# Kernel optimization log

Measured on AMD Instinct MI355X. Metric: run time of the kernel, lower is better.

Reference implementation:

```python
import jax, jax.numpy as jnp
import numpy as np

B = 64            # graphs in batch
N = 100_000       # total nodes
E = 600_000       # total edges of g == nodes of line graph lg
E2 = 1_500_000    # edges of line graph
H = 128           # hidden_dim
L = 3             # num_layers
MAXZ = 100

seg_sum = jax.ops.segment_sum


def setup_inputs() -> dict:
    key = jax.random.key(0)
    ks = jax.random.split(key, 20)
    s = 1.0 / np.sqrt(H)
    inp = {
        'z': jax.random.randint(ks[0], (N,), 0, MAXZ + 1),
        'd': jax.random.uniform(ks[1], (E, 1), dtype=jnp.float32),
        'src': jax.random.randint(ks[2], (E,), 0, N),
        'dst': jax.random.randint(ks[3], (E,), 0, N),
        'lsrc': jax.random.randint(ks[4], (E2,), 0, E),
        'ldst': jax.random.randint(ks[5], (E2,), 0, E),
        'node_graph': jnp.sort(jax.random.randint(ks[6], (N,), 0, B)),
        'edge_graph': jnp.sort(jax.random.randint(ks[7], (E,), 0, B)),
        'emb': jax.random.normal(ks[8], (MAXZ + 1, H), jnp.float32),
        'ep_w': jax.random.normal(ks[9], (1, H), jnp.float32) * s,
        'ep_b': jnp.zeros((H,), jnp.float32),
        'gW': jax.random.normal(ks[10], (L, H, H), jnp.float32) * s,
        'gb': jnp.zeros((L, H), jnp.float32),
        'lgW': jax.random.normal(ks[11], (L, H, H), jnp.float32) * s,
        'lgb': jnp.zeros((L, H), jnp.float32),
        'r1w': jax.random.normal(ks[12], (2 * H, H), jnp.float32) * s,
        'r1b': jnp.zeros((H,), jnp.float32),
        'r2w': jax.random.normal(ks[13], (H, 1), jnp.float32) * s,
        'r2b': jnp.zeros((1,), jnp.float32),
    }
    return inp


def _graph_conv(h, srcix, dstix, W, b, n_nodes):
    # DGL GraphConv, norm='both', aggregate-then-weight (in==out dims):
    # h' = D_in^{-1/2} * A^T * (D_out^{-1/2} * h) @ W + b, degrees clamped >= 1
    ones = jnp.ones(srcix.shape[0], h.dtype)
    deg_out = jnp.clip(seg_sum(ones, srcix, num_segments=n_nodes), 1.0)
    deg_in = jnp.clip(seg_sum(ones, dstix, num_segments=n_nodes), 1.0)
    m = h * (deg_out ** -0.5)[:, None]
    agg = seg_sum(m[srcix], dstix, num_segments=n_nodes)  # SpMM gather-scatter
    agg = agg * (deg_in ** -0.5)[:, None]
    return agg @ W + b


def _segment_mean(h, seg, n_seg):
    sums = seg_sum(h, seg, num_segments=n_seg)
    cnt = jnp.clip(seg_sum(jnp.ones(h.shape[0], h.dtype), seg, num_segments=n_seg), 1.0)
    return sums / cnt[:, None]


def reference(z, d, src, dst, lsrc, ldst, node_graph, edge_graph,
              emb, ep_w, ep_b, gW, gb, lgW, lgb, r1w, r1b, r2w, r2b):
    h = emb[z]                       # [N, H]
    e = d @ ep_w + ep_b              # [E, H]
    for i in range(L):
        h = jax.nn.relu(_graph_conv(h, src, dst, gW[i], gb[i], N))
    for i in range(L):
        e = jax.nn.relu(_graph_conv(e, lsrc, ldst, lgW[i], lgb[i], E))
    hg = _segment_mean(h, node_graph, B)   # [B, H]
    he = _segment_mean(e, edge_graph, B)   # [B, H]
    x = jnp.concatenate([hg, he], axis=-1)  # [B, 2H]
    y = jax.nn.silu(x @ r1w + r1b) @ r2w + r2b
    return y.reshape(-1)             # [B]
```

## Files before the change

kernel.cpp:

```cpp
#include <hip/hip_runtime.h>
#include <math.h>

#define H 128
typedef unsigned short u16;
typedef unsigned char u8;
typedef unsigned int u32;
typedef _Float16 f16;
typedef f16 f16x8 __attribute__((ext_vector_type(8)));
typedef float f32x4 __attribute__((ext_vector_type(4)));
typedef float f32x2 __attribute__((ext_vector_type(2)));

#if __has_builtin(__builtin_amdgcn_cvt_pk_fp8_f32)
#define HW8 1
#else
#define HW8 0
#endif

#define SSTRIDE 144

static inline int cdiv(long long a, long long b) { return (int)((a + b - 1) / b); }

__device__ __forceinline__ int swz_seg(int orig, int n) {
    int q = n >> 3, r = n & 7;
    int x = orig & 7;
    int base = (x < r) ? x * (q + 1) : r * (q + 1) + (x - r) * q;
    return base + (orig >> 3);
}
__device__ __forceinline__ int conv_bid(int orig, int nbCN, int nwg) {
    return (orig < nbCN) ? swz_seg(orig, nbCN)
                         : nbCN + swz_seg(orig - nbCN, nwg - nbCN);
}

struct F8 {
    static __device__ inline float dec(u8 v) {
        int e = (v >> 3) & 15, m = v & 7;
        float f = (e == 0) ? (float)m * 0.001953125f : ldexpf(1.f + 0.125f * (float)m, e - 7);
        return (v & 0x80) ? -f : f;
    }
    static __device__ inline u8 enc(float x) {
        u8 s = (u8)((__float_as_uint(x) >> 24) & 0x80);
        float ax = fabsf(x);
        if (!(ax < 448.f)) return s | 0x7E;
        if (ax < 0.015625f) {
            int m = (int)rintf(ax * 512.f);
            if (m >= 8) return s | 0x08;
            return s | (u8)m;
        }
        int e; float fr = frexpf(ax, &e);
        int E = e - 1;
        int m = (int)rintf(fr * 16.f - 8.f);
        if (m == 8) { m = 0; ++E; }
        if (E > 8) return s | 0x7E;
        return s | (u8)(((E + 7) << 3) | m);
    }
};

static __device__ inline u32 enc4(float x0, float x1, float x2, float x3) {
#if HW8
    u32 w = __builtin_amdgcn_cvt_pk_fp8_f32(x0, x1, 0, false);
    w = __builtin_amdgcn_cvt_pk_fp8_f32(x2, x3, w, true);
    return w;
#else
    union { u8 b[4]; u32 u; } p;
    p.b[0] = F8::enc(x0); p.b[1] = F8::enc(x1); p.b[2] = F8::enc(x2); p.b[3] = F8::enc(x3);
    return p.u;
#endif
}
static __device__ inline float4 dec4(u32 v) {
#if HW8
    f32x2 lo = __builtin_amdgcn_cvt_pk_f32_fp8(v, false);
    f32x2 hi = __builtin_amdgcn_cvt_pk_f32_fp8(v, true);
    return make_float4(lo.x, lo.y, hi.x, hi.y);
#else
    union { u32 u; u8 b[4]; } c; c.u = v;
    return make_float4(F8::dec(c.b[0]), F8::dec(c.b[1]), F8::dec(c.b[2]), F8::dec(c.b[3]));
#endif
}
static __device__ inline float dec1(u8 b) {
#if HW8
    return __builtin_amdgcn_cvt_f32_fp8((int)b, 0);
#else
    return F8::dec(b);
#endif
}

__global__ __launch_bounds__(256) void setup1_k(
    const float* __restrict__ gW, const float* __restrict__ lgW, f16* __restrict__ wt, int L, int nbPW,
    const int* __restrict__ src, const int* __restrict__ dst,
    const int* __restrict__ lsrc, const int* __restrict__ ldst,
    int* __restrict__ con, int* __restrict__ cin, int* __restrict__ coe, int* __restrict__ cie,
    int E, int E2, int nbHI,
    const int* __restrict__ node_graph, int N, const int* __restrict__ edge_graph,
    int B, int* __restrict__ cntn, int* __restrict__ cnte,
    const float* __restrict__ epw, const float* __restrict__ epb, float* __restrict__ uv) {
    int blk = blockIdx.x;
    if (blk < nbPW) {
        int mat = blk >> 6;
        int idx = (blk & 63) * 256 + threadIdx.x;
        int k = idx >> 7, n = idx & 127;
        const float* W = (mat < L) ? gW + (size_t)mat * H * H : lgW + (size_t)(mat - L) * H * H;
        wt[(size_t)mat * H * H + (size_t)n * H + k] = (f16)W[(size_t)k * H + n];
        return;
    }
    blk -= nbPW;
    if (blk < nbHI) {
        int i = blk * 256 + threadIdx.x;
        if (i < E) {
            atomicAdd(&con[src[i]], 1);
            atomicAdd(&cin[dst[i]], 1);
        } else if (i < E + E2) {
            int j = i - E;
            atomicAdd(&coe[lsrc[j]], 1);
            atomicAdd(&cie[ldst[j]], 1);
        }
        return;
    }
    blk -= nbHI;
    if (blk < 2) {
        const int* seg = blk ? edge_graph : node_graph;
        int n = blk ? E : N;
        int* cnt = blk ? cnte : cntn;
        __shared__ int bound[129];
        int b = threadIdx.x;
        if (b <= B) {
            int lo = 0, hi = n;
            while (lo < hi) {
                int mid = (lo + hi) >> 1;
                if (seg[mid] < b) lo = mid + 1; else hi = mid;
            }
            bound[b] = lo;
        }
        __syncthreads();
        if (b < B) cnt[b] = bound[b + 1] - bound[b];
        return;
    }
    {
        int n = threadIdx.x;
        if (n < H) {
            float su = 0.f, sv = 0.f;
            for (int k = 0; k < H; ++k) {
                float w = lgW[(size_t)k * H + n];
                su = fmaf(epw[k], w, su);
                sv = fmaf(epb[k], w, sv);
            }
            uv[n] = su;
            uv[n + H] = sv;
        }
    }
}

__global__ __launch_bounds__(256) void setup2_k(
    const int* __restrict__ con, const int* __restrict__ cin,
    const int* __restrict__ coe, const int* __restrict__ cie,
    float* __restrict__ ron, float* __restrict__ rin,
    float* __restrict__ roe, float* __restrict__ rie,
    const float* __restrict__ d, float2* __restrict__ pairE, int N, int E, int nbRS,
    int* __restrict__ offs_n, int nbN, int* __restrict__ offs_e, int* __restrict__ bsum) {
    int blk = blockIdx.x;
    if (blk < nbRS) {
        int i = blk * 256 + threadIdx.x;
        if (i < N) { int v = con[i]; ron[i] = rsqrtf((float)(v < 1 ? 1 : v)); }
        else if (i < 2 * N) { int n = i - N; int v = cin[n]; rin[n] = rsqrtf((float)(v < 1 ? 1 : v)); }
        else if (i < 2 * N + E) {
            int n = i - 2 * N; int v = coe[n];
            float r = rsqrtf((float)(v < 1 ? 1 : v));
            roe[n] = r;
            pairE[n] = make_float2(r * d[n], r);
        } else if (i < 2 * N + 2 * E) {
            int n = i - 2 * N - E; int v = cie[n]; rie[n] = rsqrtf((float)(v < 1 ? 1 : v));
        }
        return;
    }
    blk -= nbRS;
    {
        __shared__ int sh[256];
        const int* in; int* out; int n; int gid;
        if (blk < nbN) { in = cin; out = offs_n; n = N; gid = blk * 256 + threadIdx.x; }
        else { in = cie; out = offs_e; n = E; gid = (blk - nbN) * 256 + threadIdx.x; }
        int v = (gid < n) ? in[gid] : 0;
        sh[threadIdx.x] = v;
        __syncthreads();
        for (int off = 1; off < 256; off <<= 1) {
            int t = (threadIdx.x >= off) ? sh[threadIdx.x - off] : 0;
            __syncthreads();
            sh[threadIdx.x] += t;
            __syncthreads();
        }
        if (gid < n) out[gid] = sh[threadIdx.x] - v;
        if (threadIdx.x == 255) bsum[blk] = sh[255];
    }
}

__global__ __launch_bounds__(256) void scan_bsum2_k(int* __restrict__ bsum, int nbA, int nbB) {
    __shared__ int sh[256];
    __shared__ int carry;
#pragma unroll 1
    for (int part = 0; part < 2; ++part) {
        int base0 = part ? nbA : 0;
        int nb = part ? nbB : nbA;
        if (threadIdx.x == 0) carry = 0;
        __syncthreads();
        for (int base = 0; base < nb; base += 256) {
            int i = base + threadIdx.x;
            int v = (i < nb) ? bsum[base0 + i] : 0;
            sh[threadIdx.x] = v;
            __syncthreads();
            for (int off = 1; off < 256; off <<= 1) {
                int t = (threadIdx.x >= off) ? sh[threadIdx.x - off] : 0;
                __syncthreads();
                sh[threadIdx.x] += t;
                __syncthreads();
            }
            if (i < nb) bsum[base0 + i] = sh[threadIdx.x] - v + carry;
            __syncthreads();
            if (threadIdx.x == 0) carry += sh[255];
            __syncthreads();
        }
    }
}

__global__ __launch_bounds__(256) void setup3_k(
    int* __restrict__ offs_n, int* __restrict__ cur_n, int N, int nbN, int E,
    int* __restrict__ offs_e, int* __restrict__ cur_e, int E2, int nbE,
    const int* __restrict__ bsum,
    const int* __restrict__ z, const float* __restrict__ emb,
    const float* __restrict__ ron, u8* __restrict__ featN) {
    int blk = blockIdx.x;
    int nbSA = nbN + nbE;
    if (blk < nbSA) {
        int* offs; int* curp; int n; int gid; int nnz;
        if (blk < nbN) { offs = offs_n; curp = cur_n; n = N; gid = blk * 256 + threadIdx.x; nnz = E; }
        else { offs = offs_e; curp = cur_e; n = E; gid = (blk - nbN) * 256 + threadIdx.x; nnz = E2; }
        if (gid < n) {
            int v = offs[gid] + bsum[blk];
            offs[gid] = v;
            curp[gid] = v;
        }
        if (gid == 0) offs[n] = nnz;
        return;
    }
    blk -= nbSA;
    {
        int idx = blk * 256 + threadIdx.x;
        if (idx >= N * 32) return;
        int n = idx >> 5, c4 = (idx & 31) << 2;
        float sc = ron[n];
        const float4 v = *(const float4*)(emb + (size_t)z[n] * H + c4);
        *(u32*)(featN + (size_t)n * H + c4) = enc4(v.x * sc, v.y * sc, v.z * sc, v.w * sc);
    }
}

__global__ __launch_bounds__(256) void fill2_k(const int* __restrict__ src, const int* __restrict__ dst,
                                               const int* __restrict__ lsrc, const int* __restrict__ ldst,
                                               int* __restrict__ cur_n, int* __restrict__ cur_e,
                                               uint2* __restrict__ nbr_n, uint2* __restrict__ nbr_e,
                                               const float2* __restrict__ pairE, float2* __restrict__ pslot,
                                               int E, int E2) {
    int i = blockIdx.x * 256 + threadIdx.x;
    if (i < E) {
        int dd = dst[i];
        int p = atomicAdd(&cur_n[dd], 1);
        nbr_n[p] = make_uint2((u32)src[i], (u32)dd);
    } else if (i < E + E2) {
        int j = i - E;
        int ls = lsrc[j];
        int dd = ldst[j];
        int p = atomicAdd(&cur_e[dd], 1);
        nbr_e[p] = make_uint2((u32)ls, (u32)dd);
        pslot[p] = pairE[ls];
    }
}

__device__ __forceinline__ void gather_phase(
    const u8* __restrict__ Xin,
    const int* __restrict__ offs, const uint2* __restrict__ nbr2,
    const float* __restrict__ rs_in, int M,
    int row0, f16 (*As)[136], int wave, int lane) {
    const int rowbase = row0 + wave * 16;
    {
        uint2* zp = (uint2*)&As[wave * 16][0];
#pragma unroll
        for (int i = 0; i < 9; ++i) {
            int o = lane + i * 64;
            if (o < 544) zp[o] = make_uint2(0u, 0u);
        }
    }
    const int gl = lane >> 4;
    const int ln = lane & 15;
    const int rbase4 = rowbase + gl * 4;
    const int r_lo = min(rbase4, M);
    const int r_hi = min(rbase4 + 4, M);
    const int jbeg = offs[r_lo];
    const int jend = offs[r_hi];
    if (jbeg >= jend) return;
    const int mrow = M - 1;
    const float rsr0 = rs_in[min(rbase4 + 0, mrow)];
    const float rsr1 = rs_in[min(rbase4 + 1, mrow)];
    const float rsr2 = rs_in[min(rbase4 + 2, mrow)];
    const float rsr3 = rs_in[min(rbase4 + 3, mrow)];

    float a0 = 0.f, a1 = 0.f, a2 = 0.f, a3 = 0.f, a4 = 0.f, a5 = 0.f, a6 = 0.f, a7 = 0.f;
    int curdst = -1;

#define FLUSH_ROW()                                                              \
    do {                                                                         \
        const int dd_ = curdst - rbase4;                                         \
        const float ri_ = dd_ == 0 ? rsr0 : (dd_ == 1 ? rsr1 : (dd_ == 2 ? rsr2 : rsr3)); \
        f16x8 o_;                                                                \
        o_[0] = (f16)(a0 * ri_); o_[1] = (f16)(a1 * ri_);                        \
        o_[2] = (f16)(a2 * ri_); o_[3] = (f16)(a3 * ri_);                        \
        o_[4] = (f16)(a4 * ri_); o_[5] = (f16)(a5 * ri_);                        \
        o_[6] = (f16)(a6 * ri_); o_[7] = (f16)(a7 * ri_);                        \
        *(f16x8*)&As[curdst - row0][ln << 3] = o_;                               \
    } while (0)

    uint2 eA[8], eB[8], fA[8], fB[8], eN[8];
#pragma unroll
    for (int k = 0; k < 8; ++k) eA[k] = nbr2[min(jbeg + k, jend - 1)];
#pragma unroll
    for (int k = 0; k < 8; ++k) eB[k] = nbr2[min(jbeg + 8 + k, jend - 1)];
#pragma unroll
    for (int k = 0; k < 8; ++k)
        fA[k] = *(const uint2*)(Xin + ((size_t)eA[k].x << 7) + (ln << 3));
    int jc = jbeg;
    while (true) {
        const int jn = jc + 8;
        const bool more = jn < jend;
        if (more) {
#pragma unroll
            for (int k = 0; k < 8; ++k)
                fB[k] = *(const uint2*)(Xin + ((size_t)eB[k].x << 7) + (ln << 3));
#pragma unroll
            for (int k = 0; k < 8; ++k) eN[k] = nbr2[min(jn + 8 + k, jend - 1)];
        }
#pragma unroll
        for (int k = 0; k < 8; ++k) {
            if (jc + k < jend) {
                const int dk = (int)eA[k].y;
                if (dk != curdst) {
                    if (curdst >= 0) {
                        FLUSH_ROW();
                        a0 = a1 = a2 = a3 = a4 = a5 = a6 = a7 = 0.f;
                    }
                    curdst = dk;
                }
                float4 lo = dec4(fA[k].x);
                float4 hi = dec4(fA[k].y);
                a0 += lo.x; a1 += lo.y; a2 += lo.z; a3 += lo.w;
                a4 += hi.x; a5 += hi.y; a6 += hi.z; a7 += hi.w;
            }
        }
        if (!more) break;
#pragma unroll
        for (int k = 0; k < 8; ++k) { eA[k] = eB[k]; eB[k] = eN[k]; fA[k] = fB[k]; }
        jc = jn;
    }
    FLUSH_ROW();
#undef FLUSH_ROW
}

template <bool STORE>
__device__ __forceinline__ void conv_mfma_phase(
    u8* __restrict__ Xout, const f16* __restrict__ Wt, const float* __restrict__ bias,
    const float* __restrict__ scale_out, int M, int row0, f16 (*As)[136], int wave, int lane) {
    const int rowbase = row0 + wave * 16;
    if (rowbase >= M) return;
    const int l15 = lane & 15;
    const int quad = lane >> 4;

    f16x8 a[4];
#pragma unroll
    for (int kt = 0; kt < 4; ++kt)
        a[kt] = *(const f16x8*)&As[wave * 16 + l15][kt * 32 + quad * 8];

    float rsc[4];
#pragma unroll
    for (int r = 0; r < 4; ++r) {
        int gr = rowbase + quad * 4 + r;
        rsc[r] = (scale_out && gr < M) ? scale_out[gr] : 1.f;
    }

    u8* stage = (u8*)&As[wave * 16][0];

#pragma unroll
    for (int n0 = 0; n0 < 8; ++n0) {
        f32x4 acc = {0.f, 0.f, 0.f, 0.f};
        const f16* bp = Wt + (size_t)(n0 * 16 + l15) * H + quad * 8;
#pragma unroll
        for (int kt = 0; kt < 4; ++kt) {
            f16x8 b = *(const f16x8*)(bp + kt * 32);
            acc = __builtin_amdgcn_mfma_f32_16x16x32_f16(a[kt], b, acc, 0, 0, 0);
        }
        int col = n0 * 16 + l15;
        float bv = bias[col];
        float o[4];
#pragma unroll
        for (int r = 0; r < 4; ++r) o[r] = fmaxf(acc[r] + bv, 0.f) * rsc[r];
        u32 w = enc4(o[0], o[1], o[2], o[3]);
#pragma unroll
        for (int r = 0; r < 4; ++r) stage[(quad * 4 + r) * SSTRIDE + col] = (u8)(w >> (8 * r));
    }
    if (STORE) {
        const int lr = lane >> 2;
        const int lc = (lane & 3) * 32;
        int gr = rowbase + lr;
        if (gr < M) {
            uint4 v0 = *(const uint4*)&stage[lr * SSTRIDE + lc];
            uint4 v1 = *(const uint4*)&stage[lr * SSTRIDE + lc + 16];
            *(uint4*)(Xout + (size_t)gr * H + lc) = v0;
            *(uint4*)(Xout + (size_t)gr * H + lc + 16) = v1;
        }
    }
}

__device__ __forceinline__ void conv_mfma_pool_phase(
    const f16* __restrict__ Wt, const float* __restrict__ bias, int M, int row0,
    f16 (*As)[136], float (*pool)[128], int wave, int lane,
    const int* __restrict__ seg, float* __restrict__ outp, bool uni) {
    const int rowbase = row0 + wave * 16;
    if (rowbase >= M) return;
    const int l15 = lane & 15;
    const int quad = lane >> 4;

    f16x8 a[4];
#pragma unroll
    for (int kt = 0; kt < 4; ++kt)
        a[kt] = *(const f16x8*)&As[wave * 16 + l15][kt * 32 + quad * 8];

    const int gr0 = rowbase + quad * 4;
    const int remM = M - gr0;
    int g0 = -1, g1 = -1, g2 = -1, g3 = -1;
    if (!uni) {
        g0 = (0 < remM) ? seg[gr0 + 0] : -1;
        g1 = (1 < remM) ? seg[gr0 + 1] : -1;
        g2 = (2 < remM) ? seg[gr0 + 2] : -1;
        g3 = (3 < remM) ? seg[gr0 + 3] : -1;
    }

#pragma unroll
    for (int n0 = 0; n0 < 8; ++n0) {
        f32x4 acc = {0.f, 0.f, 0.f, 0.f};
        const f16* bp = Wt + (size_t)(n0 * 16 + l15) * H + quad * 8;
#pragma unroll
        for (int kt = 0; kt < 4; ++kt) {
            f16x8 b = *(const f16x8*)(bp + kt * 32);
            acc = __builtin_amdgcn_mfma_f32_16x16x32_f16(a[kt], b, acc, 0, 0, 0);
        }
        const int col = n0 * 16 + l15;
        const float bv = bias[col];
        const float o0 = (0 < remM) ? fmaxf(acc[0] + bv, 0.f) : 0.f;
        const float o1 = (1 < remM) ? fmaxf(acc[1] + bv, 0.f) : 0.f;
        const float o2 = (2 < remM) ? fmaxf(acc[2] + bv, 0.f) : 0.f;
        const float o3 = (3 < remM) ? fmaxf(acc[3] + bv, 0.f) : 0.f;
        if (uni) {
            float s = (o0 + o1) + (o2 + o3);
            s += __shfl_xor(s, 16);
            s += __shfl_xor(s, 32);
            if (quad == 0) pool[wave][col] = s;
        } else {
            float ac = o0; int gc = g0;
            if (g1 == gc) ac += o1; else { if (gc >= 0) atomicAdd(&outp[(size_t)gc * H + col], ac); gc = g1; ac = o1; }
            if (g2 == gc) ac += o2; else { if (gc >= 0) atomicAdd(&outp[(size_t)gc * H + col], ac); gc = g2; ac = o2; }
            if (g3 == gc) ac += o3; else { if (gc >= 0) atomicAdd(&outp[(size_t)gc * H + col], ac); gc = g3; ac = o3; }
            if (gc >= 0) atomicAdd(&outp[(size_t)gc * H + col], ac);
        }
    }
}

template <bool STORE>
__device__ __forceinline__ void conv_wave(
    const u8* __restrict__ Xin, u8* __restrict__ Xout,
    const int* __restrict__ offs, const uint2* __restrict__ nbr2,
    const float* __restrict__ rs_in, const f16* __restrict__ Wt,
    const float* __restrict__ bias, const float* __restrict__ scale_out, int M,
    int row0, f16 (*As)[136], int wave, int lane) {
    gather_phase(Xin, offs, nbr2, rs_in, M, row0, As, wave, lane);
    conv_mfma_phase<STORE>(Xout, Wt, bias, scale_out, M, row0, As, wave, lane);
}

__device__ __forceinline__ void conv_wave_l0e(
    u8* __restrict__ Xout, const int* __restrict__ offs,
    const float2* __restrict__ pslot, const float* __restrict__ rs_in,
    const float* __restrict__ uv, const float* __restrict__ bias,
    const float* __restrict__ scale_out, int E,
    int row0, int wave, int lane) {
    const int rowbase = row0 + wave * 16;
    const int r = lane >> 2;
    const int t = lane & 3;
    const int growu = rowbase + r;
    const int grow = min(growu, E - 1);
    const int jb = offs[grow];
    const int je = offs[grow + 1];
    float sd = 0.f, sw = 0.f;
    for (int j = jb + t; j < je; j += 4) {
        float2 p = pslot[j];
        sd += p.x; sw += p.y;
    }
    sd += __shfl_xor(sd, 1); sw += __shfl_xor(sw, 1);
    sd += __shfl_xor(sd, 2); sw += __shfl_xor(sw, 2);
    if (growu >= E) return;
    const float ri = rs_in[growu];
    const float so = scale_out[growu];
    sd *= ri; sw *= ri;
    const int c0 = t * 32;
    u32 wbuf[8];
#pragma unroll
    for (int c4 = 0; c4 < 8; ++c4) {
        const int c = c0 + c4 * 4;
        const float4 ua = *(const float4*)(uv + c);
        const float4 va = *(const float4*)(uv + H + c);
        const float4 ba = *(const float4*)(bias + c);
        const float o0 = fmaxf(fmaf(sd, ua.x, fmaf(sw, va.x, ba.x)), 0.f) * so;
        const float o1 = fmaxf(fmaf(sd, ua.y, fmaf(sw, va.y, ba.y)), 0.f) * so;
        const float o2 = fmaxf(fmaf(sd, ua.z, fmaf(sw, va.z, ba.z)), 0.f) * so;
        const float o3 = fmaxf(fmaf(sd, ua.w, fmaf(sw, va.w, ba.w)), 0.f) * so;
        wbuf[c4] = enc4(o0, o1, o2, o3);
    }
    *(uint4*)(Xout + (size_t)growu * H + c0) = *(uint4*)&wbuf[0];
    *(uint4*)(Xout + (size_t)growu * H + c0 + 16) = *(uint4*)&wbuf[4];
}

__global__ __launch_bounds__(256, 4) void conv2_k(
    const u8* __restrict__ XinN, u8* __restrict__ XoutN,
    const int* __restrict__ offs_n, const uint2* __restrict__ nbr_n,
    const float* __restrict__ rinN, const f16* __restrict__ WtN,
    const float* __restrict__ biasN, const float* __restrict__ scaleN, int N, int nbCN,
    const u8* __restrict__ XinE, u8* __restrict__ XoutE,
    const int* __restrict__ offs_e, const uint2* __restrict__ nbr_e,
    const float* __restrict__ rinE, const f16* __restrict__ WtE,
    const float* __restrict__ biasE, const float* __restrict__ scaleE, int E) {
    __shared__ f16 As[64][136];
    const int tid = threadIdx.x;
    const int wave = tid >> 6;
    const int lane = tid & 63;
    const int bid = conv_bid((int)blockIdx.x, nbCN, (int)gridDim.x);
    if (bid < nbCN) {
        conv_wave<true>(XinN, XoutN, offs_n, nbr_n, rinN, WtN, biasN, scaleN, N,
                        bid * 64, As, wave, lane);
    } else {
        conv_wave<true>(XinE, XoutE, offs_e, nbr_e, rinE, WtE, biasE, scaleE, E,
                        (bid - nbCN) * 64, As, wave, lane);
    }
}

__global__ __launch_bounds__(256, 4) void conv2_l0_k(
    const u8* __restrict__ XinN, u8* __restrict__ XoutN,
    const int* __restrict__ offs_n, const uint2* __restrict__ nbr_n,
    const float* __restrict__ rinN, const f16* __restrict__ WtN,
    const float* __restrict__ biasN, const float* __restrict__ scaleN, int N, int nbCN,
    u8* __restrict__ XoutE,
    const int* __restrict__ offs_e, const float2* __restrict__ pslot,
    const float* __restrict__ rinE, const float* __restrict__ uv,
    const float* __restrict__ biasE, const float* __restrict__ scaleE, int E) {
    __shared__ f16 As[64][136];
    const int tid = threadIdx.x;
    const int wave = tid >> 6;
    const int lane = tid & 63;
    const int bid = conv_bid((int)blockIdx.x, nbCN, (int)gridDim.x);
    if (bid < nbCN) {
        conv_wave<true>(XinN, XoutN, offs_n, nbr_n, rinN, WtN, biasN, scaleN, N,
                        bid * 64, As, wave, lane);
    } else {
        conv_wave_l0e(XoutE, offs_e, pslot, rinE, uv, biasE, scaleE, E,
                      (bid - nbCN) * 64, wave, lane);
    }
}

__global__ __launch_bounds__(256, 4) void conv2_last_k(
    const u8* __restrict__ XinN,
    const int* __restrict__ offs_n, const uint2* __restrict__ nbr_n,
    const float* __restrict__ rinN, const f16* __restrict__ WtN,
    const float* __restrict__ biasN, int N, int nbCN,
    const int* __restrict__ node_graph, float* __restrict__ hg,
    const u8* __restrict__ XinE,
    const int* __restrict__ offs_e, const uint2* __restrict__ nbr_e,
    const float* __restrict__ rinE, const f16* __restrict__ WtE,
    const float* __restrict__ biasE, int E,
    const int* __restrict__ edge_graph, float* __restrict__ he) {
    __shared__ f16 As[64][136];
    __shared__ float pool[4][128];
    const int tid = threadIdx.x;
    const int wave = tid >> 6;
    const int lane = tid & 63;
    const int bid = conv_bid((int)blockIdx.x, nbCN, (int)gridDim.x);
    const bool isN = bid < nbCN;
    const int row0 = (isN ? bid : bid - nbCN) * 64;
    const int M = isN ? N : E;
    const int* seg = isN ? node_graph : edge_graph;
    float* outp = isN ? hg : he;

    ((float*)pool)[tid] = 0.f;
    ((float*)pool)[tid + 256] = 0.f;
    const int gblk = seg[row0];
    const bool uni = (seg[min(row0 + 63, M - 1)] == gblk);
    __syncthreads();

    if (isN) {
        gather_phase(XinN, offs_n, nbr_n, rinN, N, row0, As, wave, lane);
        conv_mfma_pool_phase(WtN, biasN, N, row0, As, pool, wave, lane, seg, outp, uni);
    } else {
        gather_phase(XinE, offs_e, nbr_e, rinE, E, row0, As, wave, lane);
        conv_mfma_pool_phase(WtE, biasE, E, row0, As, pool, wave, lane, seg, outp, uni);
    }
    __syncthreads();
    if (uni && tid < 128) {
        float s = (pool[0][tid] + pool[1][tid]) + (pool[2][tid] + pool[3][tid]);
        atomicAdd(&outp[(size_t)gblk * H + tid], s);
    }
}

__global__ __launch_bounds__(128) void readout_k(const float* __restrict__ hg, const float* __restrict__ he,
                                                 const int* __restrict__ cn, const int* __restrict__ ce,
                                                 const float* __restrict__ r1w, const float* __restrict__ r1b,
                                                 const float* __restrict__ r2w, const float* __restrict__ r2b,
                                                 float* __restrict__ out) {
    const int b = blockIdx.x;
    const int j = threadIdx.x;
    const float invn = 1.f / fmaxf((float)cn[b], 1.f);
    const float inve = 1.f / fmaxf((float)ce[b], 1.f);
    float acc = r1b[j];
    for (int k = 0; k < H; ++k) acc = fmaf(hg[(size_t)b * H + k] * invn, r1w[(size_t)k * H + j], acc);
    for (int k = 0; k < H; ++k) acc = fmaf(he[(size_t)b * H + k] * inve, r1w[(size_t)(k + H) * H + j], acc);
    float s = acc / (1.f + expf(-acc));
    __shared__ float red[128];
    red[j] = s * r2w[j];
    __syncthreads();
    for (int off = 64; off > 0; off >>= 1) {
        if (j < off) red[j] += red[j + off];
        __syncthreads();
    }
    if (j == 0) out[b] = red[0] + r2b[0];
}

__global__ void report_k(float* out, int n, float val) {
    int i = blockIdx.x * 64 + threadIdx.x;
    if (i < n) out[i] = val;
}

extern "C" void kernel_launch(void* const* d_in, const int* in_sizes, int n_in,
                              void* d_out, int out_size, void* d_ws, size_t ws_size,
                              hipStream_t stream) {
    const int* z          = (const int*)d_in[0];
    const float* d        = (const float*)d_in[1];
    const int* src        = (const int*)d_in[2];
    const int* dst        = (const int*)d_in[3];
    const int* lsrc       = (const int*)d_in[4];
    const int* ldst       = (const int*)d_in[5];
    const int* node_graph = (const int*)d_in[6];
    const int* edge_graph = (const int*)d_in[7];
    const float* emb      = (const float*)d_in[8];
    const float* epw      = (const float*)d_in[9];
    const float* epb      = (const float*)d_in[10];
    const float* gW       = (const float*)d_in[11];
    const float* gb       = (const float*)d_in[12];
    const float* lgW      = (const float*)d_in[13];
    const float* lgb      = (const float*)d_in[14];
    const float* r1w      = (const float*)d_in[15];
    const float* r1b      = (const float*)d_in[16];
    const float* r2w      = (const float*)d_in[17];
    const float* r2b      = (const float*)d_in[18];

    const int N  = in_sizes[0];
    const int E  = in_sizes[2];
    const int E2 = in_sizes[4];
    const int B  = out_size;
    const int L  = 3;
    float* out = (float*)d_out;
    char* ws = (char*)d_ws;

    size_t off = 0;
    auto al = [&](size_t b) -> char* { char* q = ws + off; off += (b + 255) & ~(size_t)255; return q; };
    u8*  featEA = (u8*)al((size_t)E * H);
    u8*  featEB = (u8*)al((size_t)E * H);
    u8*  featNA = (u8*)al((size_t)N * H);
    u8*  featNB = (u8*)al((size_t)N * H);
    f16* wt    = (f16*)al((size_t)2 * L * H * H * 2);
    float* uv  = (float*)al((size_t)2 * H * 4);
    float* ron = (float*)al((size_t)N * 4);
    float* rin = (float*)al((size_t)N * 4);
    float* roe = (float*)al((size_t)E * 4);
    float* rie = (float*)al((size_t)E * 4);
    float2* pairE = (float2*)al((size_t)E * 8);
    size_t cntCount = (size_t)2 * N + 2 * E + 2 * B;
    size_t cntBytes = cntCount * 4;
    size_t poolsOff = (cntBytes + 255) & ~(size_t)255;
    char* zblock = al(poolsOff + (size_t)2 * B * H * 4);
    int* cnts = (int*)zblock;
    float* pools = (float*)(zblock + poolsOff);
    int* con = cnts; int* cin_ = con + N; int* coe = cin_ + N; int* cie = coe + E;
    int* cntn = cie + E; int* cnte = cntn + B;
    float* hg = pools;
    float* he = pools + (size_t)B * H;
    int* offs_n = (int*)al(((size_t)N + 1) * 4);
    int* cur_n  = (int*)al((size_t)N * 4);
    int* offs_e = (int*)al(((size_t)E + 1) * 4);
    int* cur_e  = (int*)al((size_t)E * 4);
    uint2* nbr_n = (uint2*)al((size_t)E * 8);
    uint2* nbr_e = (uint2*)al((size_t)E2 * 8);
    float2* pslot = (float2*)al((size_t)E2 * 8);
    int nbN = cdiv(N, 256), nbE = cdiv(E, 256);
    int* bsum   = (int*)al(((size_t)nbN + nbE + 2) * 4);

    if (off > ws_size) {
        report_k<<<cdiv(B, 64), 64, 0, stream>>>(out, B, (float)(ws_size >> 20));
        return;
    }

    hipMemsetAsync(zblock, 0, poolsOff + (size_t)2 * B * H * 4, stream);

    const int nbPW = 2 * L * 64;
    const int nbHI = cdiv((long long)E + E2, 256);
    setup1_k<<<nbPW + nbHI + 3, 256, 0, stream>>>(gW, lgW, wt, L, nbPW,
                                                  src, dst, lsrc, ldst, con, cin_, coe, cie,
                                                  E, E2, nbHI, node_graph, N, edge_graph, B, cntn, cnte,
                                                  epw, epb, uv);

    const int nbRS = cdiv((long long)2 * N + 2 * E, 256);
    setup2_k<<<nbRS + nbN + nbE, 256, 0, stream>>>(con, cin_, coe, cie, ron, rin, roe, rie,
                                                   d, pairE, N, E, nbRS, offs_n, nbN, offs_e, bsum);
    scan_bsum2_k<<<1, 256, 0, stream>>>(bsum, nbN, nbE);

    const int nbIN = cdiv((long long)N * 32, 256);
    setup3_k<<<nbN + nbE + nbIN, 256, 0, stream>>>(offs_n, cur_n, N, nbN, E,
                                                   offs_e, cur_e, E2, nbE, bsum, z, emb, ron, featNA);

    fill2_k<<<cdiv((long long)E + E2, 256), 256, 0, stream>>>(src, dst, lsrc, ldst, cur_n, cur_e,
                                                              nbr_n, nbr_e, pairE, pslot, E, E2);

    const int nbCN = cdiv(N, 64), nbCE = cdiv(E, 64);

    conv2_l0_k<<<nbCN + nbCE, 256, 0, stream>>>(
        featNA, featNB, offs_n, nbr_n, rin, wt, gb, ron, N, nbCN,
        featEB, offs_e, pslot, rie, uv, lgb, roe, E);

    conv2_k<<<nbCN + nbCE, 256, 0, stream>>>(
        featNB, featNA, offs_n, nbr_n, rin, wt + (size_t)1 * H * H, gb + (size_t)1 * H, ron, N, nbCN,
        featEB, featEA, offs_e, nbr_e, rie, wt + (size_t)(L + 1) * H * H, lgb + (size_t)1 * H, roe, E);

    conv2_last_k<<<nbCN + nbCE, 256, 0, stream>>>(
        featNA, offs_n, nbr_n, rin, wt + (size_t)2 * H * H, gb + (size_t)2 * H, N, nbCN, node_graph, hg,
        featEA, offs_e, nbr_e, rie, wt + (size_t)(L + 2) * H * H, lgb + (size_t)2 * H, E, edge_graph, he);

    readout_k<<<B, 128, 0, stream>>>(hg, he, cntn, cnte, r1w, r1b, r2w, r2b, out);
}
```

Measured before the change: 1.012 ms.

## Stage SpMM neighbor gathers through LDS with async global_load_lds pipeline

Rewrites the gather phase so each wave handles 16 rows together rather than 4 rows per 16-lane group. Neighbor index chunks and fp8 feature rows are copied straight into a per-wave LDS staging buffer with global_load_lds, using a 4-deep ring and explicit vmcnt waits to keep loads in flight. Each lane then accumulates 2 channels and flushes through a shuffle of the row scale. The aim is better memory-level parallelism and lower register pressure in the gather, at the cost of about 20KB extra LDS per block, which may reduce occupancy, plus serialized per-edge processing across the wave.

New measurement: 1.074 ms. 6.1% more time.

```diff
diff --git a/kernel.cpp b/kernel.cpp
--- a/kernel.cpp
+++ b/kernel.cpp
@@ -10,6 +10,9 @@
 typedef float f32x4 __attribute__((ext_vector_type(4)));
 typedef float f32x2 __attribute__((ext_vector_type(2)));
 
+typedef __attribute__((address_space(1))) const void gas_void;
+typedef __attribute__((address_space(3))) void las_void;
+
 #if __has_builtin(__builtin_amdgcn_cvt_pk_fp8_f32)
 #define HW8 1
 #else
@@ -17,6 +20,7 @@
 #endif
 
 #define SSTRIDE 144
+#define STG_W 5120
 
 static inline int cdiv(long long a, long long b) { return (int)((a + b - 1) / b); }
 
@@ -74,13 +78,6 @@
 #else
     union { u32 u; u8 b[4]; } c; c.u = v;
     return make_float4(F8::dec(c.b[0]), F8::dec(c.b[1]), F8::dec(c.b[2]), F8::dec(c.b[3]));
-#endif
-}
-static __device__ inline float dec1(u8 b) {
-#if HW8
-    return __builtin_amdgcn_cvt_f32_fp8((int)b, 0);
-#else
-    return F8::dec(b);
 #endif
 }
 
@@ -274,8 +271,8 @@
 __device__ __forceinline__ void gather_phase(
     const u8* __restrict__ Xin,
     const int* __restrict__ offs, const uint2* __restrict__ nbr2,
-    const float* __restrict__ rs_in, int M,
-    int row0, f16 (*As)[136], int wave, int lane) {
+    const float* __restrict__ rs_in, int M, int nnz,
+    int row0, f16 (*As)[136], u8* __restrict__ stageW, int wave, int lane) {
     const int rowbase = row0 + wave * 16;
     {
         uint2* zp = (uint2*)&As[wave * 16][0];
@@ -285,78 +282,80 @@
             if (o < 544) zp[o] = make_uint2(0u, 0u);
         }
     }
-    const int gl = lane >> 4;
-    const int ln = lane & 15;
-    const int rbase4 = rowbase + gl * 4;
-    const int r_lo = min(rbase4, M);
-    const int r_hi = min(rbase4 + 4, M);
-    const int jbeg = offs[r_lo];
-    const int jend = offs[r_hi];
-    if (jbeg >= jend) return;
-    const int mrow = M - 1;
-    const float rsr0 = rs_in[min(rbase4 + 0, mrow)];
-    const float rsr1 = rs_in[min(rbase4 + 1, mrow)];
-    const float rsr2 = rs_in[min(rbase4 + 2, mrow)];
-    const float rsr3 = rs_in[min(rbase4 + 3, mrow)];
-
-    float a0 = 0.f, a1 = 0.f, a2 = 0.f, a3 = 0.f, a4 = 0.f, a5 = 0.f, a6 = 0.f, a7 = 0.f;
+    if (rowbase >= M) return;
+    const int rhi = min(rowbase + 16, M);
+    const int J0 = offs[rowbase];
+    const int J1 = offs[rhi];
+    if (J0 >= J1) return;
+
+    float rsv = rs_in[min(rowbase + (lane & 15), M - 1)];
+    asm volatile("" : "+v"(rsv));
+
+    u8* featW = stageW;
+    int* nbrW = (int*)(stageW + 4096);
+
+    float acc0 = 0.f, acc1 = 0.f;
     int curdst = -1;
 
-#define FLUSH_ROW()                                                              \
+#define FLUSH()                                                                  \
     do {                                                                         \
-        const int dd_ = curdst - rbase4;                                         \
-        const float ri_ = dd_ == 0 ? rsr0 : (dd_ == 1 ? rsr1 : (dd_ == 2 ? rsr2 : rsr3)); \
-        f16x8 o_;                                                                \
-        o_[0] = (f16)(a0 * ri_); o_[1] = (f16)(a1 * ri_);                        \
-        o_[2] = (f16)(a2 * ri_); o_[3] = (f16)(a3 * ri_);                        \
-        o_[4] = (f16)(a4 * ri_); o_[5] = (f16)(a5 * ri_);                        \
-        o_[6] = (f16)(a6 * ri_); o_[7] = (f16)(a7 * ri_);                        \
-        *(f16x8*)&As[curdst - row0][ln << 3] = o_;                               \
+        float ri_ = __shfl(rsv, curdst - rowbase);                               \
+        union { f16 h[2]; u32 u; } P_;                                           \
+        P_.h[0] = (f16)(acc0 * ri_);                                             \
+        P_.h[1] = (f16)(acc1 * ri_);                                             \
+        *((u32*)&As[curdst - row0][0] + lane) = P_.u;                            \
     } while (0)
 
-    uint2 eA[8], eB[8], fA[8], fB[8], eN[8];
-#pragma unroll
-    for (int k = 0; k < 8; ++k) eA[k] = nbr2[min(jbeg + k, jend - 1)];
-#pragma unroll
-    for (int k = 0; k < 8; ++k) eB[k] = nbr2[min(jbeg + 8 + k, jend - 1)];
-#pragma unroll
-    for (int k = 0; k < 8; ++k)
-        fA[k] = *(const uint2*)(Xin + ((size_t)eA[k].x << 7) + (ln << 3));
-    int jc = jbeg;
-    while (true) {
-        const int jn = jc + 8;
-        const bool more = jn < jend;
-        if (more) {
-#pragma unroll
-            for (int k = 0; k < 8; ++k)
-                fB[k] = *(const uint2*)(Xin + ((size_t)eB[k].x << 7) + (ln << 3));
-#pragma unroll
-            for (int k = 0; k < 8; ++k) eN[k] = nbr2[min(jn + 8 + k, jend - 1)];
-        }
-#pragma unroll
-        for (int k = 0; k < 8; ++k) {
-            if (jc + k < jend) {
-                const int dk = (int)eA[k].y;
-                if (dk != curdst) {
-                    if (curdst >= 0) {
-                        FLUSH_ROW();
-                        a0 = a1 = a2 = a3 = a4 = a5 = a6 = a7 = 0.f;
+#define STAGE(t)                                                                 \
+    do {                                                                         \
+        int ce_ = min((t) * 8 + (lane >> 3), nb - 1);                            \
+        u32 sn_ = (u32)nbrW[ce_ * 2];                                            \
+        const u8* g_ = Xin + ((size_t)sn_ << 7) + ((size_t)(lane & 7) << 4);     \
+        __builtin_amdgcn_global_load_lds((gas_void*)g_,                          \
+            (las_void*)(featW + ((t) & 3) * 1024), 16, 0, 0);                    \
+    } while (0)
+
+    for (int C = J0; C < J1; C += 128) {
+        const int nb = min(J1 - C, 128);
+        {
+            int ce = min(C + 2 * lane, nnz - 1);
+            const u8* g = (const u8*)(nbr2 + ce);
+            __builtin_amdgcn_global_load_lds((gas_void*)g, (las_void*)nbrW, 16, 0, 0);
+        }
+        asm volatile("s_waitcnt vmcnt(0)" ::: "memory");
+        __builtin_amdgcn_sched_barrier(0);
+        const int nbat = (nb + 7) >> 3;
+        STAGE(0); STAGE(1); STAGE(2);
+        for (int b = 0; b < nbat; ++b) {
+            asm volatile("s_waitcnt vmcnt(2)" ::: "memory");
+            __builtin_amdgcn_sched_barrier(0);
+            STAGE(b + 3);
+            const u8* fb = featW + (b & 3) * 1024;
+#pragma unroll
+            for (int k = 0; k < 8; ++k) {
+                const int kk = b * 8 + k;
+                if (kk < nb) {
+                    int dk = __builtin_amdgcn_readfirstlane(nbrW[kk * 2 + 1]);
+                    if (dk != curdst) {
+                        if (curdst >= 0) FLUSH();
+                        acc0 = 0.f; acc1 = 0.f;
+                        curdst = dk;
                     }
-                    curdst = dk;
+                    u32 w = *(const u16*)(fb + k * 128 + (lane << 1));
+#if HW8
+                    f32x2 d2 = __builtin_amdgcn_cvt_pk_f32_fp8((int)w, false);
+                    acc0 += d2.x; acc1 += d2.y;
+#else
+                    acc0 += F8::dec((u8)(w & 255));
+                    acc1 += F8::dec((u8)(w >> 8));
+#endif
                 }
-                float4 lo = dec4(fA[k].x);
-                float4 hi = dec4(fA[k].y);
-                a0 += lo.x; a1 += lo.y; a2 += lo.z; a3 += lo.w;
-                a4 += hi.x; a5 += hi.y; a6 += hi.z; a7 += hi.w;
             }
         }
-        if (!more) break;
-#pragma unroll
-        for (int k = 0; k < 8; ++k) { eA[k] = eB[k]; eB[k] = eN[k]; fA[k] = fB[k]; }
-        jc = jn;
-    }
-    FLUSH_ROW();
-#undef FLUSH_ROW
+    }
+    if (curdst >= 0) FLUSH();
+#undef STAGE
+#undef FLUSH
 }
 
 template <bool STORE>
@@ -472,9 +471,9 @@
     const u8* __restrict__ Xin, u8* __restrict__ Xout,
     const int* __restrict__ offs, const uint2* __restrict__ nbr2,
     const float* __restrict__ rs_in, const f16* __restrict__ Wt,
-    const float* __restrict__ bias, const float* __restrict__ scale_out, int M,
-    int row0, f16 (*As)[136], int wave, int lane) {
-    gather_phase(Xin, offs, nbr2, rs_in, M, row0, As, wave, lane);
+    const float* __restrict__ bias, const float* __restrict__ scale_out, int M, int nnz,
+    int row0, f16 (*As)[136], u8* __restrict__ stageW, int wave, int lane) {
+    gather_phase(Xin, offs, nbr2, rs_in, M, nnz, row0, As, stageW, wave, lane);
     conv_mfma_phase<STORE>(Xout, Wt, bias, scale_out, M, row0, As, wave, lane);
 }
 
@@ -528,18 +527,19 @@
     const u8* __restrict__ XinE, u8* __restrict__ XoutE,
     const int* __restrict__ offs_e, const uint2* __restrict__ nbr_e,
     const float* __restrict__ rinE, const f16* __restrict__ WtE,
-    const float* __restrict__ biasE, const float* __restrict__ scaleE, int E) {
+    const float* __restrict__ biasE, const float* __restrict__ scaleE, int E, int E2) {
     __shared__ f16 As[64][136];
+    __shared__ u8 Stg[4][STG_W];
     const int tid = threadIdx.x;
     const int wave = tid >> 6;
     const int lane = tid & 63;
     const int bid = conv_bid((int)blockIdx.x, nbCN, (int)gridDim.x);
     if (bid < nbCN) {
-        conv_wave<true>(XinN, XoutN, offs_n, nbr_n, rinN, WtN, biasN, scaleN, N,
-                        bid * 64, As, wave, lane);
+        conv_wave<true>(XinN, XoutN, offs_n, nbr_n, rinN, WtN, biasN, scaleN, N, E,
+                        bid * 64, As, Stg[wave], wave, lane);
     } else {
-        conv_wave<true>(XinE, XoutE, offs_e, nbr_e, rinE, WtE, biasE, scaleE, E,
-                        (bid - nbCN) * 64, As, wave, lane);
+        conv_wave<true>(XinE, XoutE, offs_e, nbr_e, rinE, WtE, biasE, scaleE, E, E2,
+                        (bid - nbCN) * 64, As, Stg[wave], wave, lane);
     }
 }
 
@@ -553,13 +553,14 @@
     const float* __restrict__ rinE, const float* __restrict__ uv,
     const float* __restrict__ biasE, const float* __restrict__ scaleE, int E) {
     __shared__ f16 As[64][136];
+    __shared__ u8 Stg[4][STG_W];
     const int tid = threadIdx.x;
     const int wave = tid >> 6;
     const int lane = tid & 63;
     const int bid = conv_bid((int)blockIdx.x, nbCN, (int)gridDim.x);
     if (bid < nbCN) {
-        conv_wave<true>(XinN, XoutN, offs_n, nbr_n, rinN, WtN, biasN, scaleN, N,
-                        bid * 64, As, wave, lane);
+        conv_wave<true>(XinN, XoutN, offs_n, nbr_n, rinN, WtN, biasN, scaleN, N, E,
+                        bid * 64, As, Stg[wave], wave, lane);
     } else {
         conv_wave_l0e(XoutE, offs_e, pslot, rinE, uv, biasE, scaleE, E,
                       (bid - nbCN) * 64, wave, lane);
@@ -575,9 +576,10 @@
     const u8* __restrict__ XinE,
     const int* __restrict__ offs_e, const uint2* __restrict__ nbr_e,
     const float* __restrict__ rinE, const f16* __restrict__ WtE,
-    const float* __restrict__ biasE, int E,
+    const float* __restrict__ biasE, int E, int E2,
     const int* __restrict__ edge_graph, float* __restrict__ he) {
     __shared__ f16 As[64][136];
+    __shared__ u8 Stg[4][STG_W];
     __shared__ float pool[4][128];
     const int tid = threadIdx.x;
     const int wave = tid >> 6;
@@ -596,10 +598,10 @@
     __syncthreads();
 
     if (isN) {
-        gather_phase(XinN, offs_n, nbr_n, rinN, N, row0, As, wave, lane);
+        gather_phase(XinN, offs_n, nbr_n, rinN, N, E, row0, As, Stg[wave], wave, lane);
         conv_mfma_pool_phase(WtN, biasN, N, row0, As, pool, wave, lane, seg, outp, uni);
     } else {
-        gather_phase(XinE, offs_e, nbr_e, rinE, E, row0, As, wave, lane);
+        gather_phase(XinE, offs_e, nbr_e, rinE, E, E2, row0, As, Stg[wave], wave, lane);
         conv_mfma_pool_phase(WtE, biasE, E, row0, As, pool, wave, lane, seg, outp, uni);
     }
     __syncthreads();
@@ -735,11 +737,11 @@
 
     conv2_k<<<nbCN + nbCE, 256, 0, stream>>>(
         featNB, featNA, offs_n, nbr_n, rin, wt + (size_t)1 * H * H, gb + (size_t)1 * H, ron, N, nbCN,
-        featEB, featEA, offs_e, nbr_e, rie, wt + (size_t)(L + 1) * H * H, lgb + (size_t)1 * H, roe, E);
+        featEB, featEA, offs_e, nbr_e, rie, wt + (size_t)(L + 1) * H * H, lgb + (size_t)1 * H, roe, E, E2);
 
     conv2_last_k<<<nbCN + nbCE, 256, 0, stream>>>(
         featNA, offs_n, nbr_n, rin, wt + (size_t)2 * H * H, gb + (size_t)2 * H, N, nbCN, node_graph, hg,
-        featEA, offs_e, nbr_e, rie, wt + (size_t)(L + 2) * H * H, lgb + (size_t)2 * H, E, edge_graph, he);
+        featEA, offs_e, nbr_e, rie, wt + (size_t)(L + 2) * H * H, lgb + (size_t)2 * H, E, E2, edge_graph, he);
 
     readout_k<<<B, 128, 0, stream>>>(hg, he, cntn, cnte, r1w, r1b, r2w, r2b, out);
 }
```
